# Kernel optimization log

Measured on AMD Instinct MI355X. Metric: run time of the kernel, lower is better.

The kernel has to match this reference:

```python
import jax, jax.numpy as jnp
import numpy as np

B, N, C = 8, 2048, 64  # batch, num nodes, channels
DENSITY = 0.01


def setup_inputs() -> dict:
    key = jax.random.key(0)
    k = jax.random.split(key, 8)
    x = jax.random.normal(k[0], (B, N, C), dtype=jnp.float32)

    # --- replicate sym_norm_Adj(Adj_matrix) + row softmax from __init__ ---
    W = (jax.random.uniform(k[1], (N, N)) < DENSITY).astype(jnp.float32)
    W = W + 0.5 * jnp.eye(N, dtype=jnp.float32)          # W + 0.5*I
    deg = jnp.sum((W != 0.0).astype(jnp.float32), axis=1)  # row nonzero counts
    A = jnp.sqrt(deg)[:, None] * W * jnp.sqrt(deg)[None, :]  # sqrt(D) W sqrt(D)
    A = jax.nn.softmax(A, axis=1)

    s = 1.0 / np.sqrt(C)
    Wq = jax.random.normal(k[2], (C, C), dtype=jnp.float32) * s   # stored as (in,out)
    Wk = jax.random.normal(k[3], (C, C), dtype=jnp.float32) * s
    Wv = jax.random.normal(k[4], (C, N), dtype=jnp.float32) * s   # c_in -> num_node
    theta_w = jax.random.normal(k[5], (C, C), dtype=jnp.float32) * s
    theta_b = jnp.zeros((C,), dtype=jnp.float32)
    alpha = jnp.array([0.95], dtype=jnp.float32)
    beta = jnp.array([0.95], dtype=jnp.float32)
    return {"x": x, "A": A, "Wq": Wq, "Wk": Wk, "Wv": Wv,
            "theta_w": theta_w, "theta_b": theta_b, "alpha": alpha, "beta": beta}


def reference(x, A, Wq, Wk, Wv, theta_w, theta_b, alpha, beta):
    # Spatial_Attention_layer
    Q = x @ Wq                                   # (B,N,C)
    K = x @ Wk                                   # (B,N,C)
    V = x @ Wv                                   # (B,N,N)
    score = jnp.einsum('bnc,bmc->bnm', Q, K)     # (B,N,N)
    score = jax.nn.softmax(score, axis=1)        # softmax over dim=1 (as in torch code)
    spat = jnp.einsum('bnm,bmk->bnk', score, V)  # (B,N,N) spatial attention

    # einsum('nn,bnc->bnc', A, x) == diag(A) broadcast-multiply
    static_out = jnp.diagonal(A)[None, :, None] * x  # (B,N,C)

    # dy_adj = A @ spat; einsum('bnn,bnc->bnc', dy_adj, x) uses only diag(dy_adj)
    dy_diag = jnp.einsum('nj,bjn->bn', A, spat)      # (B,N), avoids (B,N,N) intermediate
    dy_out = (dy_diag[:, :, None] * x) @ theta_w + theta_b  # Theta1 linear

    out = jax.nn.relu(alpha[0] * static_out + beta[0] * dy_out)
    return out
```

## Files before the change

kernel.cpp:

```cpp
#include <hip/hip_runtime.h>

constexpr int Bb = 8;
constexpr int Nn = 2048;
constexpr int Cc = 64;
constexpr int CAPS = 192;

typedef __attribute__((ext_vector_type(4))) float f32x4;
typedef __attribute__((ext_vector_type(8))) short bf16x8;

__device__ inline unsigned short f2bf(float f){
  unsigned u = __builtin_bit_cast(unsigned, f);
  unsigned r = (u + 0x7FFFu + ((u>>16)&1u)) >> 16;
  return (unsigned short)r;
}
__device__ inline float bf2f(unsigned short h){
  unsigned u = ((unsigned)h)<<16; return __builtin_bit_cast(float,u);
}

__global__ __launch_bounds__(256) void mega_k(
    const float* __restrict__ x, const float* __restrict__ A,
    const float* __restrict__ Wq, const float* __restrict__ Wk,
    const float* __restrict__ Tw, const float* __restrict__ Wv,
    unsigned short* __restrict__ Qhi, unsigned short* __restrict__ Qlo,
    unsigned short* __restrict__ Khi, unsigned short* __restrict__ Klo,
    float* __restrict__ xt, float* __restrict__ Xp,
    float* __restrict__ r_, float* __restrict__ diagA, int* __restrict__ cnt,
    int* __restrict__ idx, float* __restrict__ val,
    float* __restrict__ WvT, char* __restrict__ zerobase){
  __shared__ __attribute__((aligned(16))) char smem[65792];
  int blk = blockIdx.x; int t = threadIdx.x;

  if(blk < 256){
    float* wql = (float*)smem;
    float* wkl = wql + 4096;
    float* twl = wkl + 4096;
    float (*xr)[64] = (float(*)[64])(twl + 4096);
    float* xsl = (float*)(xr + 64);
    #pragma unroll
    for(int i=0;i<4;i++){
      *(f32x4*)&wql[i*1024+t*4] = *(const f32x4*)&Wq[i*1024+t*4];
      *(f32x4*)&wkl[i*1024+t*4] = *(const f32x4*)&Wk[i*1024+t*4];
      *(f32x4*)&twl[i*1024+t*4] = *(const f32x4*)&Tw[i*1024+t*4];
    }
    if(t<64) xsl[t]=0.f;
    long long row0 = (long long)blk*64;
    int r = t>>4, q = t&15, c0 = q*4;
    #pragma unroll
    for(int i=0;i<4;i++){
      int row = i*16 + r;
      *(f32x4*)&xr[row][c0] = *(const f32x4*)&x[(row0+row)*Cc + c0];
    }
    __syncthreads();
    f32x4 aq[4], ak[4], at4[4];
    #pragma unroll
    for(int g=0;g<4;g++){ aq[g]=(f32x4){0,0,0,0}; ak[g]=(f32x4){0,0,0,0}; at4[g]=(f32x4){0,0,0,0}; }
    for(int kk=0;kk<64;kk++){
      f32x4 wq4 = *(const f32x4*)&wql[kk*64+c0];
      f32x4 wk4 = *(const f32x4*)&wkl[kk*64+c0];
      f32x4 wt4 = *(const f32x4*)&twl[kk*64+c0];
      #pragma unroll
      for(int g=0;g<4;g++){
        float xv = xr[g*16+r][kk];
        aq[g] += xv*wq4; ak[g] += xv*wk4; at4[g] += xv*wt4;
      }
    }
    float xsp[4] = {0.f,0.f,0.f,0.f};
    #pragma unroll
    for(int g=0;g<4;g++){
      #pragma unroll
      for(int d=0;d<4;d++) xsp[d] += xr[g*16+r][c0+d];
      long long g2 = (row0 + g*16 + r)*Cc + c0;
      unsigned long long hq=0,lq=0,hk=0,lk=0;
      #pragma unroll
      for(int d=0;d<4;d++){
        float v = aq[g][d];
        unsigned short h = f2bf(v); unsigned short lo2 = f2bf(v - bf2f(h));
        hq |= (unsigned long long)h << (16*d); lq |= (unsigned long long)lo2 << (16*d);
        v = ak[g][d];
        h = f2bf(v); lo2 = f2bf(v - bf2f(h));
        hk |= (unsigned long long)h << (16*d); lk |= (unsigned long long)lo2 << (16*d);
      }
      *(unsigned long long*)&Qhi[g2] = hq;
      *(unsigned long long*)&Qlo[g2] = lq;
      *(unsigned long long*)&Khi[g2] = hk;
      *(unsigned long long*)&Klo[g2] = lk;
      *(f32x4*)&xt[g2] = at4[g];
    }
    __syncthreads();
    #pragma unroll
    for(int d=0;d<4;d++) atomicAdd(&xsl[c0+d], xsp[d]);
    __syncthreads();
    if(t<64) Xp[blk*64+t] = xsl[t];
  } else if(blk < 768){
    int n = (blk-256)*4 + (t>>6); int l = t&63;
    const float* row = A + (size_t)n*Nn;
    float mn = 1e30f;
    for(int j=l;j<Nn;j+=64) mn = fminf(mn, row[j]);
    #pragma unroll
    for(int off=32;off>=1;off>>=1) mn = fminf(mn, __shfl_xor(mn,off));
    float thr = mn*1.3f;
    int bse=0;
    for(int j0=0;j0<Nn;j0+=64){
      float v = row[j0+l];
      bool f = v>thr;
      unsigned long long m = __ballot(f);
      int pos = __popcll(m & ((1ull<<l)-1ull));
      if(f && bse+pos<CAPS){ idx[n*CAPS+bse+pos]=j0+l; val[n*CAPS+bse+pos]=v-mn; }
      bse += __popcll(m);
    }
    if(l==0){ r_[n]=mn; diagA[n]=row[n]; cnt[n] = bse<CAPS? bse : CAPS; }
  } else if(blk < 800){
    float (*tile)[65] = (float(*)[65])smem;
    int n0 = (blk-768)*64;
    for(int i=0;i<16;i++){
      int cc = i*4 + (t>>6); int nn2 = t&63;
      tile[cc][nn2] = Wv[(size_t)cc*Nn + n0 + nn2];
    }
    __syncthreads();
    for(int i=0;i<16;i++){
      int nn2 = i*4 + (t>>6); int cc = t&63;
      WvT[(size_t)(n0+nn2)*Cc + cc] = tile[cc][nn2];
    }
  } else {
    char* dst = zerobase + (size_t)(blk-800)*65536;
    uint4 zz = {0,0,0,0};
    #pragma unroll
    for(int i=0;i<16;i++) *(uint4*)(dst + ((size_t)i*256 + t)*16) = zz;
  }
}

__device__ inline void stage_tile128(uint4* __restrict__ ldsT,
                                     const unsigned short* __restrict__ g, int t){
  #pragma unroll
  for(int i=0;i<4;i++){
    int t2 = i*256+t; int row = t2>>3, ch = t2&7;
    uint4 v = *(const uint4*)(g + row*Cc + ch*8);
    ldsT[row*8 + (ch^(row&7))] = v;
  }
}

__global__ __launch_bounds__(256) void gemm1_k(
    const unsigned short* __restrict__ Qhi, const unsigned short* __restrict__ Qlo,
    const unsigned short* __restrict__ Khi, const unsigned short* __restrict__ Klo,
    unsigned short* __restrict__ E, float* __restrict__ Z){
  __shared__ uint4 lds[4*128*8];
  __shared__ float colsum[128];
  int t = threadIdx.x;
  int b = blockIdx.z;
  int j0 = blockIdx.x*128, m0 = blockIdx.y*128;
  size_t bq = ((size_t)b*Nn + j0)*Cc;
  size_t bk = ((size_t)b*Nn + m0)*Cc;
  uint4* qh=lds; uint4* ql=lds+1024; uint4* kh=lds+2048; uint4* kl=lds+3072;
  stage_tile128(qh, Qhi+bq, t);
  stage_tile128(ql, Qlo+bq, t);
  stage_tile128(kh, Khi+bk, t);
  stage_tile128(kl, Klo+bk, t);
  if(t<128) colsum[t]=0.f;
  __syncthreads();
  int w=t>>6, l=t&63;
  int wm=(w>>1)*64, wn=(w&1)*64;
  f32x4 acc[4][4];
  #pragma unroll
  for(int i=0;i<4;i++)
    #pragma unroll
    for(int j=0;j<4;j++) acc[i][j]=(f32x4){0.f,0.f,0.f,0.f};
  #pragma unroll
  for(int ks=0;ks<2;ks++){
    bf16x8 ah[4],al2[4],bh[4],bl[4];
    #pragma unroll
    for(int i=0;i<4;i++){
      int R = wm+i*16+(l&15); int ch=(ks*4+(l>>4))^(R&7);
      ah[i]=*(bf16x8*)&qh[R*8+ch];
      al2[i]=*(bf16x8*)&ql[R*8+ch];
      int Rb= wn+i*16+(l&15); int cb=(ks*4+(l>>4))^(Rb&7);
      bh[i]=*(bf16x8*)&kh[Rb*8+cb];
      bl[i]=*(bf16x8*)&kl[Rb*8+cb];
    }
    #pragma unroll
    for(int i=0;i<4;i++)
      #pragma unroll
      for(int j=0;j<4;j++){
        acc[i][j]=__builtin_amdgcn_mfma_f32_16x16x32_bf16(ah[i],bh[j],acc[i][j],0,0,0);
        acc[i][j]=__builtin_amdgcn_mfma_f32_16x16x32_bf16(al2[i],bh[j],acc[i][j],0,0,0);
        acc[i][j]=__builtin_amdgcn_mfma_f32_16x16x32_bf16(ah[i],bl[j],acc[i][j],0,0,0);
      }
  }
  unsigned short* Eb = E + ((size_t)b*Nn + j0)*Nn + m0;
  float cs[4] = {0.f,0.f,0.f,0.f};
  #pragma unroll
  for(int i=0;i<4;i++){
    int row = wm+i*16+(l>>4)*4;
    #pragma unroll
    for(int j=0;j<4;j++){
      int col = wn+j*16+(l&15);
      #pragma unroll
      for(int q=0;q<4;q++){
        unsigned short h = f2bf(__expf(acc[i][j][q]));
        Eb[(size_t)(row+q)*Nn + col] = h;
        cs[j] += bf2f(h);
      }
    }
  }
  #pragma unroll
  for(int j=0;j<4;j++)
    atomicAdd(&colsum[wn + j*16 + (l&15)], cs[j]);
  __syncthreads();
  if(t<128) atomicAdd(&Z[(size_t)b*Nn + m0 + t], colsum[t]);
}

__global__ __launch_bounds__(256) void xzt_k(const float* __restrict__ x,
    const float* __restrict__ Z, unsigned short* __restrict__ xzT){
  __shared__ float tile[64][65];
  int b = blockIdx.y;
  int m0 = blockIdx.x*64; int t = threadIdx.x;
  for(int i=0;i<16;i++){
    int mm = i*4 + (t>>6); int cc = t&63;
    tile[mm][cc] = x[((size_t)b*Nn + m0+mm)*Cc + cc];
  }
  __syncthreads();
  for(int i=0;i<16;i++){
    int cc = i*4 + (t>>6); int mm = t&63;
    float iz = 1.0f/Z[(size_t)b*Nn + m0+mm];
    xzT[((size_t)b*Cc + cc)*Nn + m0 + mm] = f2bf(tile[mm][cc]*iz);
  }
}

__global__ __launch_bounds__(256) void gemm2_k(const unsigned short* __restrict__ E,
    const unsigned short* __restrict__ xzT, float* __restrict__ P){
  __shared__ uint4 et[128*16];
  __shared__ uint4 xb[64*16];
  int t = threadIdx.x;
  int b = blockIdx.z;
  int j0 = blockIdx.x*128;
  int kc = blockIdx.y;
  int w = t>>6, l = t&63;
  f32x4 acc[2][4];
  #pragma unroll
  for(int i=0;i<2;i++)
    #pragma unroll
    for(int j=0;j<4;j++) acc[i][j]=(f32x4){0.f,0.f,0.f,0.f};
  const unsigned short* Ebase = E + ((size_t)b*Nn + j0)*Nn;
  const unsigned short* Xbase = xzT + (size_t)b*Cc*Nn;
  for(int it=0; it<4; it++){
    int m0 = kc*512 + it*128;
    #pragma unroll
    for(int i=0;i<8;i++){
      int t2=i*256+t; int row=t2>>4, ch=t2&15;
      et[row*16 + (ch^(row&15))] = *(const uint4*)(Ebase + (size_t)row*Nn + m0 + ch*8);
    }
    #pragma unroll
    for(int i=0;i<4;i++){
      int t2=i*256+t; int row=t2>>4, ch=t2&15;
      xb[row*16 + (ch^(row&15))] = *(const uint4*)(Xbase + (size_t)row*Nn + m0 + ch*8);
    }
    __syncthreads();
    #pragma unroll
    for(int ks=0;ks<4;ks++){
      bf16x8 af[2], bfr[4];
      #pragma unroll
      for(int i=0;i<2;i++){
        int R = w*32 + i*16 + (l&15); int ch=(ks*4+(l>>4))^(R&15);
        af[i] = *(bf16x8*)&et[R*16+ch];
      }
      #pragma unroll
      for(int j=0;j<4;j++){
        int R = j*16 + (l&15); int ch=(ks*4+(l>>4))^(R&15);
        bfr[j] = *(bf16x8*)&xb[R*16+ch];
      }
      #pragma unroll
      for(int i=0;i<2;i++)
        #pragma unroll
        for(int j=0;j<4;j++)
          acc[i][j] = __builtin_amdgcn_mfma_f32_16x16x32_bf16(af[i],bfr[j],acc[i][j],0,0,0);
    }
    __syncthreads();
  }
  float* Pb = P + ((size_t)b*Nn + j0)*Cc;
  #pragma unroll
  for(int i=0;i<2;i++){
    int row = w*32 + i*16 + (l>>4)*4;
    #pragma unroll
    for(int j=0;j<4;j++){
      int col = j*16 + (l&15);
      #pragma unroll
      for(int q=0;q<4;q++)
        atomicAdd(&Pb[(size_t)(row+q)*Cc + col], acc[i][j][q]);
    }
  }
}

__global__ __launch_bounds__(256) void final_k(const float* __restrict__ x,
    const float* __restrict__ xt, const float* __restrict__ P,
    const float* __restrict__ WvT, const float* __restrict__ Xp,
    const float* __restrict__ r_, const float* __restrict__ diagA,
    const int* __restrict__ cnt, const int* __restrict__ idx,
    const float* __restrict__ val, const float* __restrict__ tb,
    const float* __restrict__ alp, const float* __restrict__ bet,
    float* __restrict__ out){
  int t=threadIdx.x; int l=t&63;
  int bn = blockIdx.x*4 + (t>>6);
  int b = bn>>11, n = bn&2047;
  float wv = WvT[n*Cc+l];
  float xs = 0.f;
  const float* xpb = Xp + (size_t)b*32*Cc;
  #pragma unroll 8
  for(int p=0;p<32;p++) xs += xpb[p*Cc + l];
  float tacc = r_[n]*xs;
  int cn = cnt[n];
  const float* Pb = P + (size_t)b*Nn*Cc;
  const int* ix = idx + n*CAPS;
  const float* vl = val + n*CAPS;
  for(int k=0;k<cn;k++)
    tacc += vl[k] * Pb[(size_t)ix[k]*Cc + l];
  float d = wv*tacc;
  #pragma unroll
  for(int off=32;off>=1;off>>=1) d += __shfl_xor(d,off);
  size_t g = (size_t)bn*Cc + l;
  float o = alp[0]*diagA[n]*x[g] + bet[0]*(d*xt[g] + tb[l]);
  out[g] = fmaxf(o,0.f);
}

extern "C" void kernel_launch(void* const* d_in, const int* in_sizes, int n_in,
                              void* d_out, int out_size, void* d_ws, size_t ws_size,
                              hipStream_t stream){
  const float* x  = (const float*)d_in[0];
  const float* A  = (const float*)d_in[1];
  const float* Wq = (const float*)d_in[2];
  const float* Wk = (const float*)d_in[3];
  const float* Wv = (const float*)d_in[4];
  const float* Tw = (const float*)d_in[5];
  const float* tb = (const float*)d_in[6];
  const float* alp= (const float*)d_in[7];
  const float* bet= (const float*)d_in[8];
  float* out = (float*)d_out;

  char* base = (char*)d_ws; size_t off=0;
  auto al=[&](size_t sz)->void*{ void* q = base+off; off=(off+sz+255)&~(size_t)255; return q; };
  unsigned short* Qhi=(unsigned short*)al((size_t)Bb*Nn*Cc*2);
  unsigned short* Qlo=(unsigned short*)al((size_t)Bb*Nn*Cc*2);
  unsigned short* Khi=(unsigned short*)al((size_t)Bb*Nn*Cc*2);
  unsigned short* Klo=(unsigned short*)al((size_t)Bb*Nn*Cc*2);
  float* xt  =(float*)al((size_t)Bb*Nn*Cc*4);
  float* P   =(float*)al((size_t)Bb*Nn*Cc*4);
  float* Z   =(float*)al((size_t)Bb*Nn*4);
  float* Xp  =(float*)al((size_t)256*Cc*4);
  float* WvT =(float*)al((size_t)Nn*Cc*4);
  float* r_  =(float*)al((size_t)Nn*4);
  float* dgA =(float*)al((size_t)Nn*4);
  int*   cnt =(int*)al((size_t)Nn*4);
  int*   idx =(int*)al((size_t)Nn*CAPS*4);
  float* val =(float*)al((size_t)Nn*CAPS*4);
  unsigned short* xzT=(unsigned short*)al((size_t)Bb*Cc*Nn*2);
  unsigned short* E  =(unsigned short*)al((size_t)Bb*Nn*Nn*2);
  (void)ws_size;

  mega_k<<<865, 256, 0, stream>>>(x, A, Wq, Wk, Tw, Wv,
      Qhi, Qlo, Khi, Klo, xt, Xp, r_, dgA, cnt, idx, val, WvT, (char*)P);
  gemm1_k<<<dim3(16,16,Bb), 256, 0, stream>>>(Qhi,Qlo,Khi,Klo,E,Z);
  xzt_k<<<dim3(32,Bb), 256, 0, stream>>>(x,Z,xzT);
  gemm2_k<<<dim3(16,4,Bb), 256, 0, stream>>>(E,xzT,P);
  final_k<<<Bb*Nn/4, 256, 0, stream>>>(x,xt,P,WvT,Xp,r_,dgA,cnt,idx,val,tb,alp,bet,out);
}
```

Before: 128.7 us.

## Load GEMM operands directly from global memory and preswizzle xzT for LDS staging

gemm1 no longer stages Q/K hi/lo tiles in LDS; each wave loads its MFMA fragments straight from global memory. gemm2 now loads the whole 64x512 xzT slab into LDS once, with xzT written in an XOR-swizzled layout by xzt_k. E fragments are read directly from global memory with a two-stage register double buffer, which removes the per-iteration barriers. The aim is to cut LDS traffic and syncs, at the cost of relying on L1/L2 for the redundant global fragment reads and of less coalesced access.

```diff
diff --git a/kernel.cpp b/kernel.cpp
--- a/kernel.cpp
+++ b/kernel.cpp
@@ -129,36 +129,24 @@
   }
 }
 
-__device__ inline void stage_tile128(uint4* __restrict__ ldsT,
-                                     const unsigned short* __restrict__ g, int t){
-  #pragma unroll
-  for(int i=0;i<4;i++){
-    int t2 = i*256+t; int row = t2>>3, ch = t2&7;
-    uint4 v = *(const uint4*)(g + row*Cc + ch*8);
-    ldsT[row*8 + (ch^(row&7))] = v;
-  }
-}
-
 __global__ __launch_bounds__(256) void gemm1_k(
     const unsigned short* __restrict__ Qhi, const unsigned short* __restrict__ Qlo,
     const unsigned short* __restrict__ Khi, const unsigned short* __restrict__ Klo,
     unsigned short* __restrict__ E, float* __restrict__ Z){
-  __shared__ uint4 lds[4*128*8];
   __shared__ float colsum[128];
   int t = threadIdx.x;
   int b = blockIdx.z;
   int j0 = blockIdx.x*128, m0 = blockIdx.y*128;
+  int w=t>>6, l=t&63;
+  int wm=(w>>1)*64, wn=(w&1)*64;
+  if(t<128) colsum[t]=0.f;
+  __syncthreads();
   size_t bq = ((size_t)b*Nn + j0)*Cc;
   size_t bk = ((size_t)b*Nn + m0)*Cc;
-  uint4* qh=lds; uint4* ql=lds+1024; uint4* kh=lds+2048; uint4* kl=lds+3072;
-  stage_tile128(qh, Qhi+bq, t);
-  stage_tile128(ql, Qlo+bq, t);
-  stage_tile128(kh, Khi+bk, t);
-  stage_tile128(kl, Klo+bk, t);
-  if(t<128) colsum[t]=0.f;
-  __syncthreads();
-  int w=t>>6, l=t&63;
-  int wm=(w>>1)*64, wn=(w&1)*64;
+  const unsigned short* qhB = Qhi + bq;
+  const unsigned short* qlB = Qlo + bq;
+  const unsigned short* khB = Khi + bk;
+  const unsigned short* klB = Klo + bk;
   f32x4 acc[4][4];
   #pragma unroll
   for(int i=0;i<4;i++)
@@ -166,15 +154,16 @@
     for(int j=0;j<4;j++) acc[i][j]=(f32x4){0.f,0.f,0.f,0.f};
   #pragma unroll
   for(int ks=0;ks<2;ks++){
+    int co = ks*32 + (l>>4)*8;
     bf16x8 ah[4],al2[4],bh[4],bl[4];
     #pragma unroll
     for(int i=0;i<4;i++){
-      int R = wm+i*16+(l&15); int ch=(ks*4+(l>>4))^(R&7);
-      ah[i]=*(bf16x8*)&qh[R*8+ch];
-      al2[i]=*(bf16x8*)&ql[R*8+ch];
-      int Rb= wn+i*16+(l&15); int cb=(ks*4+(l>>4))^(Rb&7);
-      bh[i]=*(bf16x8*)&kh[Rb*8+cb];
-      bl[i]=*(bf16x8*)&kl[Rb*8+cb];
+      size_t ra = (size_t)(wm+i*16+(l&15))*Cc + co;
+      ah[i]  = *(const bf16x8*)(qhB + ra);
+      al2[i] = *(const bf16x8*)(qlB + ra);
+      size_t rb = (size_t)(wn+i*16+(l&15))*Cc + co;
+      bh[i]  = *(const bf16x8*)(khB + rb);
+      bl[i]  = *(const bf16x8*)(klB + rb);
     }
     #pragma unroll
     for(int i=0;i<4;i++)
@@ -220,61 +209,72 @@
   __syncthreads();
   for(int i=0;i<16;i++){
     int cc = i*4 + (t>>6); int mm = t&63;
-    float iz = 1.0f/Z[(size_t)b*Nn + m0+mm];
-    xzT[((size_t)b*Cc + cc)*Nn + m0 + mm] = f2bf(tile[mm][cc]*iz);
+    int mabs = m0 + mm;
+    float iz = 1.0f/Z[(size_t)b*Nn + mabs];
+    int cmp = (mabs>>3) ^ (cc&7);
+    size_t pos = ((size_t)b*Cc + cc)*Nn + ((size_t)cmp<<3) + (mabs&7);
+    xzT[pos] = f2bf(tile[mm][cc]*iz);
   }
 }
 
 __global__ __launch_bounds__(256) void gemm2_k(const unsigned short* __restrict__ E,
     const unsigned short* __restrict__ xzT, float* __restrict__ P){
-  __shared__ uint4 et[128*16];
-  __shared__ uint4 xb[64*16];
+  __shared__ uint4 xb[4096];
   int t = threadIdx.x;
   int b = blockIdx.z;
   int j0 = blockIdx.x*128;
   int kc = blockIdx.y;
+  {
+    const uint4* src = (const uint4*)(xzT + (size_t)b*Cc*Nn) + kc*64;
+    #pragma unroll
+    for(int i=0;i<16;i++){
+      int idx2 = i*256+t; int row = idx2>>6, col = idx2&63;
+      xb[idx2] = src[(size_t)row*256 + col];
+    }
+  }
+  __syncthreads();
   int w = t>>6, l = t&63;
+  const unsigned short* Er0 = E + ((size_t)b*Nn + j0 + w*32      + (l&15))*Nn + kc*512 + (l>>4)*8;
+  const unsigned short* Er1 = E + ((size_t)b*Nn + j0 + w*32 + 16 + (l&15))*Nn + kc*512 + (l>>4)*8;
+  int cbase = (l&15)*64;
+  int sw = l&7;
+  int ch0 = (l>>4);
   f32x4 acc[2][4];
   #pragma unroll
   for(int i=0;i<2;i++)
     #pragma unroll
     for(int j=0;j<4;j++) acc[i][j]=(f32x4){0.f,0.f,0.f,0.f};
-  const unsigned short* Ebase = E + ((size_t)b*Nn + j0)*Nn;
-  const unsigned short* Xbase = xzT + (size_t)b*Cc*Nn;
-  for(int it=0; it<4; it++){
-    int m0 = kc*512 + it*128;
-    #pragma unroll
-    for(int i=0;i<8;i++){
-      int t2=i*256+t; int row=t2>>4, ch=t2&15;
-      et[row*16 + (ch^(row&15))] = *(const uint4*)(Ebase + (size_t)row*Nn + m0 + ch*8);
-    }
-    #pragma unroll
-    for(int i=0;i<4;i++){
-      int t2=i*256+t; int row=t2>>4, ch=t2&15;
-      xb[row*16 + (ch^(row&15))] = *(const uint4*)(Xbase + (size_t)row*Nn + m0 + ch*8);
-    }
-    __syncthreads();
-    #pragma unroll
-    for(int ks=0;ks<4;ks++){
-      bf16x8 af[2], bfr[4];
-      #pragma unroll
-      for(int i=0;i<2;i++){
-        int R = w*32 + i*16 + (l&15); int ch=(ks*4+(l>>4))^(R&15);
-        af[i] = *(bf16x8*)&et[R*16+ch];
-      }
-      #pragma unroll
-      for(int j=0;j<4;j++){
-        int R = j*16 + (l&15); int ch=(ks*4+(l>>4))^(R&15);
-        bfr[j] = *(bf16x8*)&xb[R*16+ch];
-      }
-      #pragma unroll
-      for(int i=0;i<2;i++)
-        #pragma unroll
-        for(int j=0;j<4;j++)
-          acc[i][j] = __builtin_amdgcn_mfma_f32_16x16x32_bf16(af[i],bfr[j],acc[i][j],0,0,0);
-    }
-    __syncthreads();
-  }
+
+  bf16x8 Aa0,Aa1,Ab0,Ab1,Ab2,Ab3;
+  bf16x8 Ba0,Ba1,Bb0,Bb1,Bb2,Bb3;
+#define LDF(P0,P1,Q0,Q1,Q2,Q3,st) { \
+    int mo = (st)*32; int c4 = (st)*4 + ch0; \
+    P0 = *(const bf16x8*)(Er0 + mo); \
+    P1 = *(const bf16x8*)(Er1 + mo); \
+    Q0 = *(bf16x8*)&xb[cbase        + (c4^sw)]; \
+    Q1 = *(bf16x8*)&xb[cbase + 1024 + (c4^sw)]; \
+    Q2 = *(bf16x8*)&xb[cbase + 2048 + (c4^sw)]; \
+    Q3 = *(bf16x8*)&xb[cbase + 3072 + (c4^sw)]; }
+#define MM(P0,P1,Q0,Q1,Q2,Q3) { \
+    acc[0][0]=__builtin_amdgcn_mfma_f32_16x16x32_bf16(P0,Q0,acc[0][0],0,0,0); \
+    acc[0][1]=__builtin_amdgcn_mfma_f32_16x16x32_bf16(P0,Q1,acc[0][1],0,0,0); \
+    acc[0][2]=__builtin_amdgcn_mfma_f32_16x16x32_bf16(P0,Q2,acc[0][2],0,0,0); \
+    acc[0][3]=__builtin_amdgcn_mfma_f32_16x16x32_bf16(P0,Q3,acc[0][3],0,0,0); \
+    acc[1][0]=__builtin_amdgcn_mfma_f32_16x16x32_bf16(P1,Q0,acc[1][0],0,0,0); \
+    acc[1][1]=__builtin_amdgcn_mfma_f32_16x16x32_bf16(P1,Q1,acc[1][1],0,0,0); \
+    acc[1][2]=__builtin_amdgcn_mfma_f32_16x16x32_bf16(P1,Q2,acc[1][2],0,0,0); \
+    acc[1][3]=__builtin_amdgcn_mfma_f32_16x16x32_bf16(P1,Q3,acc[1][3],0,0,0); }
+
+  LDF(Aa0,Aa1,Ab0,Ab1,Ab2,Ab3, 0);
+  #pragma unroll
+  for(int s2=0; s2<16; s2+=2){
+    if(s2+1<16) LDF(Ba0,Ba1,Bb0,Bb1,Bb2,Bb3, s2+1);
+    MM(Aa0,Aa1,Ab0,Ab1,Ab2,Ab3);
+    if(s2+2<16) LDF(Aa0,Aa1,Ab0,Ab1,Ab2,Ab3, s2+2);
+    if(s2+1<16) MM(Ba0,Ba1,Bb0,Bb1,Bb2,Bb3);
+  }
+#undef LDF
+#undef MM
   float* Pb = P + ((size_t)b*Nn + j0)*Cc;
   #pragma unroll
   for(int i=0;i<2;i++){
```

Measured after the change: 138.1 us. 1.07x slower.

## Recompute exp scores in fused attention GEMM instead of materializing E matrix

Applied to the files above, without the earlier changes.

Removes the bf16 exp(score) matrix E (B*N*N, 64 MB) from global memory. A first pass now only computes column sums Z with 32x32 MFMAs, and the second GEMM recomputes QK^T and exp on the fly. It packs the results into MFMA operands via v_permlane32_swap, then multiplies by xzT. This trades the E write and read traffic for doubled QK^T MFMA and exp work, with operands loaded straight from global memory without LDS staging. Z accumulation no longer rounds exp to bf16 before summing, so it differs slightly from the E values that get multiplied.

```diff
diff --git a/kernel.cpp b/kernel.cpp
--- a/kernel.cpp
+++ b/kernel.cpp
@@ -6,7 +6,9 @@
 constexpr int CAPS = 192;
 
 typedef __attribute__((ext_vector_type(4))) float f32x4;
+typedef __attribute__((ext_vector_type(16))) float f32x16;
 typedef __attribute__((ext_vector_type(8))) short bf16x8;
+typedef __attribute__((ext_vector_type(4))) unsigned u32x4;
 
 __device__ inline unsigned short f2bf(float f){
   unsigned u = __builtin_bit_cast(unsigned, f);
@@ -16,6 +18,11 @@
 __device__ inline float bf2f(unsigned short h){
   unsigned u = ((unsigned)h)<<16; return __builtin_bit_cast(float,u);
 }
+__device__ inline unsigned pk2(float a, float b){
+  return (unsigned)f2bf(a) | ((unsigned)f2bf(b)<<16);
+}
+
+#define MFMA32(a,b,c) __builtin_amdgcn_mfma_f32_32x32x16_bf16(a,b,c,0,0,0)
 
 __global__ __launch_bounds__(256) void mega_k(
     const float* __restrict__ x, const float* __restrict__ A,
@@ -129,83 +136,46 @@
   }
 }
 
-__device__ inline void stage_tile128(uint4* __restrict__ ldsT,
-                                     const unsigned short* __restrict__ g, int t){
-  #pragma unroll
-  for(int i=0;i<4;i++){
-    int t2 = i*256+t; int row = t2>>3, ch = t2&7;
-    uint4 v = *(const uint4*)(g + row*Cc + ch*8);
-    ldsT[row*8 + (ch^(row&7))] = v;
-  }
-}
-
-__global__ __launch_bounds__(256) void gemm1_k(
+__global__ __launch_bounds__(256) void zpass_k(
     const unsigned short* __restrict__ Qhi, const unsigned short* __restrict__ Qlo,
     const unsigned short* __restrict__ Khi, const unsigned short* __restrict__ Klo,
-    unsigned short* __restrict__ E, float* __restrict__ Z){
-  __shared__ uint4 lds[4*128*8];
-  __shared__ float colsum[128];
-  int t = threadIdx.x;
+    float* __restrict__ Z){
+  int t = threadIdx.x, w = t>>6, l = t&63, lr = l&31, hh = l>>5;
   int b = blockIdx.z;
-  int j0 = blockIdx.x*128, m0 = blockIdx.y*128;
-  size_t bq = ((size_t)b*Nn + j0)*Cc;
-  size_t bk = ((size_t)b*Nn + m0)*Cc;
-  uint4* qh=lds; uint4* ql=lds+1024; uint4* kh=lds+2048; uint4* kl=lds+3072;
-  stage_tile128(qh, Qhi+bq, t);
-  stage_tile128(ql, Qlo+bq, t);
-  stage_tile128(kh, Khi+bk, t);
-  stage_tile128(kl, Klo+bk, t);
-  if(t<128) colsum[t]=0.f;
-  __syncthreads();
-  int w=t>>6, l=t&63;
-  int wm=(w>>1)*64, wn=(w&1)*64;
-  f32x4 acc[4][4];
-  #pragma unroll
-  for(int i=0;i<4;i++)
-    #pragma unroll
-    for(int j=0;j<4;j++) acc[i][j]=(f32x4){0.f,0.f,0.f,0.f};
-  #pragma unroll
-  for(int ks=0;ks<2;ks++){
-    bf16x8 ah[4],al2[4],bh[4],bl[4];
-    #pragma unroll
-    for(int i=0;i<4;i++){
-      int R = wm+i*16+(l&15); int ch=(ks*4+(l>>4))^(R&7);
-      ah[i]=*(bf16x8*)&qh[R*8+ch];
-      al2[i]=*(bf16x8*)&ql[R*8+ch];
-      int Rb= wn+i*16+(l&15); int cb=(ks*4+(l>>4))^(Rb&7);
-      bh[i]=*(bf16x8*)&kh[Rb*8+cb];
-      bl[i]=*(bf16x8*)&kl[Rb*8+cb];
-    }
-    #pragma unroll
-    for(int i=0;i<4;i++)
-      #pragma unroll
-      for(int j=0;j<4;j++){
-        acc[i][j]=__builtin_amdgcn_mfma_f32_16x16x32_bf16(ah[i],bh[j],acc[i][j],0,0,0);
-        acc[i][j]=__builtin_amdgcn_mfma_f32_16x16x32_bf16(al2[i],bh[j],acc[i][j],0,0,0);
-        acc[i][j]=__builtin_amdgcn_mfma_f32_16x16x32_bf16(ah[i],bl[j],acc[i][j],0,0,0);
+  int j0 = blockIdx.x*128 + (w>>1)*64;
+  int m0 = blockIdx.y*128 + (w&1)*64;
+  const unsigned short* qb  = Qhi + ((size_t)b*Nn + j0 + lr)*Cc + hh*8;
+  const unsigned short* qlb = Qlo + ((size_t)b*Nn + j0 + lr)*Cc + hh*8;
+  const unsigned short* kb  = Khi + ((size_t)b*Nn + m0 + lr)*Cc + hh*8;
+  const unsigned short* klb = Klo + ((size_t)b*Nn + m0 + lr)*Cc + hh*8;
+  #pragma unroll
+  for(int mm=0; mm<2; mm++){
+    bf16x8 Bh[4], Bl[4];
+    #pragma unroll
+    for(int s=0;s<4;s++){
+      Bh[s] = *(const bf16x8*)(kb  + (size_t)mm*32*Cc + s*16);
+      Bl[s] = *(const bf16x8*)(klb + (size_t)mm*32*Cc + s*16);
+    }
+    float part = 0.f;
+    #pragma unroll
+    for(int jj=0;jj<2;jj++){
+      f32x16 sa;
+      #pragma unroll
+      for(int r=0;r<16;r++) sa[r]=0.f;
+      #pragma unroll
+      for(int s=0;s<4;s++){
+        bf16x8 Ah = *(const bf16x8*)(qb  + (size_t)jj*32*Cc + s*16);
+        bf16x8 Al = *(const bf16x8*)(qlb + (size_t)jj*32*Cc + s*16);
+        sa = MFMA32(Ah,Bh[s],sa);
+        sa = MFMA32(Al,Bh[s],sa);
+        sa = MFMA32(Ah,Bl[s],sa);
       }
-  }
-  unsigned short* Eb = E + ((size_t)b*Nn + j0)*Nn + m0;
-  float cs[4] = {0.f,0.f,0.f,0.f};
-  #pragma unroll
-  for(int i=0;i<4;i++){
-    int row = wm+i*16+(l>>4)*4;
-    #pragma unroll
-    for(int j=0;j<4;j++){
-      int col = wn+j*16+(l&15);
-      #pragma unroll
-      for(int q=0;q<4;q++){
-        unsigned short h = f2bf(__expf(acc[i][j][q]));
-        Eb[(size_t)(row+q)*Nn + col] = h;
-        cs[j] += bf2f(h);
-      }
-    }
-  }
-  #pragma unroll
-  for(int j=0;j<4;j++)
-    atomicAdd(&colsum[wn + j*16 + (l&15)], cs[j]);
-  __syncthreads();
-  if(t<128) atomicAdd(&Z[(size_t)b*Nn + m0 + t], colsum[t]);
+      #pragma unroll
+      for(int r=0;r<16;r++) part += __expf(sa[r]);
+    }
+    part += __shfl_down(part, 32);
+    if(l<32) atomicAdd(&Z[(size_t)b*Nn + m0 + mm*32 + l], part);
+  }
 }
 
 __global__ __launch_bounds__(256) void xzt_k(const float* __restrict__ x,
@@ -225,67 +195,77 @@
   }
 }
 
-__global__ __launch_bounds__(256) void gemm2_k(const unsigned short* __restrict__ E,
+__global__ __launch_bounds__(256) void fused_k(
+    const unsigned short* __restrict__ Qhi, const unsigned short* __restrict__ Qlo,
+    const unsigned short* __restrict__ Khi, const unsigned short* __restrict__ Klo,
     const unsigned short* __restrict__ xzT, float* __restrict__ P){
-  __shared__ uint4 et[128*16];
-  __shared__ uint4 xb[64*16];
-  int t = threadIdx.x;
+  int t = threadIdx.x, w = t>>6, l = t&63, lr = l&31, hh = l>>5;
   int b = blockIdx.z;
-  int j0 = blockIdx.x*128;
+  int j0 = blockIdx.x*128 + w*32;
   int kc = blockIdx.y;
-  int w = t>>6, l = t&63;
-  f32x4 acc[2][4];
-  #pragma unroll
-  for(int i=0;i<2;i++)
-    #pragma unroll
-    for(int j=0;j<4;j++) acc[i][j]=(f32x4){0.f,0.f,0.f,0.f};
-  const unsigned short* Ebase = E + ((size_t)b*Nn + j0)*Nn;
-  const unsigned short* Xbase = xzT + (size_t)b*Cc*Nn;
-  for(int it=0; it<4; it++){
-    int m0 = kc*512 + it*128;
-    #pragma unroll
-    for(int i=0;i<8;i++){
-      int t2=i*256+t; int row=t2>>4, ch=t2&15;
-      et[row*16 + (ch^(row&15))] = *(const uint4*)(Ebase + (size_t)row*Nn + m0 + ch*8);
-    }
-    #pragma unroll
-    for(int i=0;i<4;i++){
-      int t2=i*256+t; int row=t2>>4, ch=t2&15;
-      xb[row*16 + (ch^(row&15))] = *(const uint4*)(Xbase + (size_t)row*Nn + m0 + ch*8);
-    }
-    __syncthreads();
-    #pragma unroll
-    for(int ks=0;ks<4;ks++){
-      bf16x8 af[2], bfr[4];
-      #pragma unroll
-      for(int i=0;i<2;i++){
-        int R = w*32 + i*16 + (l&15); int ch=(ks*4+(l>>4))^(R&15);
-        af[i] = *(bf16x8*)&et[R*16+ch];
-      }
-      #pragma unroll
-      for(int j=0;j<4;j++){
-        int R = j*16 + (l&15); int ch=(ks*4+(l>>4))^(R&15);
-        bfr[j] = *(bf16x8*)&xb[R*16+ch];
-      }
-      #pragma unroll
-      for(int i=0;i<2;i++)
-        #pragma unroll
-        for(int j=0;j<4;j++)
-          acc[i][j] = __builtin_amdgcn_mfma_f32_16x16x32_bf16(af[i],bfr[j],acc[i][j],0,0,0);
-    }
-    __syncthreads();
+  const unsigned short* qb  = Qhi + ((size_t)b*Nn + j0 + lr)*Cc + hh*8;
+  const unsigned short* qlb = Qlo + ((size_t)b*Nn + j0 + lr)*Cc + hh*8;
+  bf16x8 Qh[4], Ql[4];
+  #pragma unroll
+  for(int s=0;s<4;s++){
+    Qh[s] = *(const bf16x8*)(qb  + s*16);
+    Ql[s] = *(const bf16x8*)(qlb + s*16);
+  }
+  const unsigned short* kb  = Khi + ((size_t)b*Nn + lr)*Cc + hh*8;
+  const unsigned short* klb = Klo + ((size_t)b*Nn + lr)*Cc + hh*8;
+  const unsigned short* xzb = xzT + ((size_t)b*Cc + lr)*Nn + hh*8;
+  f32x16 pa0, pa1;
+  #pragma unroll
+  for(int r=0;r<16;r++){ pa0[r]=0.f; pa1[r]=0.f; }
+  int mend = kc*512 + 512;
+  for(int m0 = kc*512; m0 < mend; m0 += 32){
+    f32x16 sa;
+    #pragma unroll
+    for(int r=0;r<16;r++) sa[r]=0.f;
+    #pragma unroll
+    for(int s=0;s<4;s++){
+      bf16x8 Ah = *(const bf16x8*)(kb  + (size_t)m0*Cc + s*16);
+      bf16x8 Al = *(const bf16x8*)(klb + (size_t)m0*Cc + s*16);
+      sa = MFMA32(Ah, Qh[s], sa);
+      sa = MFMA32(Al, Qh[s], sa);
+      sa = MFMA32(Ah, Ql[s], sa);
+    }
+    unsigned wd0,wd1,wd2,wd3,wd4,wd5,wd6,wd7;
+    {
+      unsigned x0 = pk2(__expf(sa[0]),  __expf(sa[1]));
+      unsigned x1 = pk2(__expf(sa[2]),  __expf(sa[3]));
+      unsigned y0 = pk2(__expf(sa[4]),  __expf(sa[5]));
+      unsigned y1 = pk2(__expf(sa[6]),  __expf(sa[7]));
+      asm("v_permlane32_swap_b32 %0, %1" : "+v"(x0), "+v"(y0));
+      asm("v_permlane32_swap_b32 %0, %1" : "+v"(x1), "+v"(y1));
+      wd0=x0; wd1=x1; wd2=y0; wd3=y1;
+      unsigned x2 = pk2(__expf(sa[8]),  __expf(sa[9]));
+      unsigned x3 = pk2(__expf(sa[10]), __expf(sa[11]));
+      unsigned y2 = pk2(__expf(sa[12]), __expf(sa[13]));
+      unsigned y3 = pk2(__expf(sa[14]), __expf(sa[15]));
+      asm("v_permlane32_swap_b32 %0, %1" : "+v"(x2), "+v"(y2));
+      asm("v_permlane32_swap_b32 %0, %1" : "+v"(x3), "+v"(y3));
+      wd4=x2; wd5=x3; wd6=y2; wd7=y3;
+    }
+    u32x4 u1 = {wd0,wd1,wd2,wd3};
+    u32x4 u2 = {wd4,wd5,wd6,wd7};
+    bf16x8 f1 = __builtin_bit_cast(bf16x8, u1);
+    bf16x8 f2 = __builtin_bit_cast(bf16x8, u2);
+    bf16x8 b00 = *(const bf16x8*)(xzb + m0);
+    bf16x8 b01 = *(const bf16x8*)(xzb + m0 + 16);
+    bf16x8 b10 = *(const bf16x8*)(xzb + (size_t)32*Nn + m0);
+    bf16x8 b11 = *(const bf16x8*)(xzb + (size_t)32*Nn + m0 + 16);
+    pa0 = MFMA32(f1, b00, pa0);
+    pa0 = MFMA32(f2, b01, pa0);
+    pa1 = MFMA32(f1, b10, pa1);
+    pa1 = MFMA32(f2, b11, pa1);
   }
   float* Pb = P + ((size_t)b*Nn + j0)*Cc;
   #pragma unroll
-  for(int i=0;i<2;i++){
-    int row = w*32 + i*16 + (l>>4)*4;
-    #pragma unroll
-    for(int j=0;j<4;j++){
-      int col = j*16 + (l&15);
-      #pragma unroll
-      for(int q=0;q<4;q++)
-        atomicAdd(&Pb[(size_t)(row+q)*Cc + col], acc[i][j][q]);
-    }
+  for(int r=0;r<16;r++){
+    int jr = (r&3) + 8*(r>>2) + 4*hh;
+    atomicAdd(&Pb[(size_t)jr*Cc + lr],      pa0[r]);
+    atomicAdd(&Pb[(size_t)jr*Cc + 32 + lr], pa1[r]);
   }
 }
 
@@ -351,13 +331,12 @@
   int*   idx =(int*)al((size_t)Nn*CAPS*4);
   float* val =(float*)al((size_t)Nn*CAPS*4);
   unsigned short* xzT=(unsigned short*)al((size_t)Bb*Cc*Nn*2);
-  unsigned short* E  =(unsigned short*)al((size_t)Bb*Nn*Nn*2);
   (void)ws_size;
 
   mega_k<<<865, 256, 0, stream>>>(x, A, Wq, Wk, Tw, Wv,
       Qhi, Qlo, Khi, Klo, xt, Xp, r_, dgA, cnt, idx, val, WvT, (char*)P);
-  gemm1_k<<<dim3(16,16,Bb), 256, 0, stream>>>(Qhi,Qlo,Khi,Klo,E,Z);
+  zpass_k<<<dim3(16,16,Bb), 256, 0, stream>>>(Qhi,Qlo,Khi,Klo,Z);
   xzt_k<<<dim3(32,Bb), 256, 0, stream>>>(x,Z,xzT);
-  gemm2_k<<<dim3(16,4,Bb), 256, 0, stream>>>(E,xzT,P);
+  fused_k<<<dim3(16,4,Bb), 256, 0, stream>>>(Qhi,Qlo,Khi,Klo,xzT,P);
   final_k<<<Bb*Nn/4, 256, 0, stream>>>(x,xt,P,WvT,Xp,r_,dgA,cnt,idx,val,tb,alp,bet,out);
 }
```

New measurement: 170.4 us. 32.4% more time.
